# Performance work log

Measured on AMD Instinct MI355X. Metric: run time of the kernel, lower is better.

The kernel has to match this reference:

```python
import jax, jax.numpy as jnp
import numpy as np

BIT, ROW, COL = 4, 8, 8
Y_ROW, Z_COL, K = 128, 128, 256  # inter_dimension = 256, K8 = 32
K8 = K // 8
BATCH, SEQ = 8, 2048


def _unpack_bits(packed, n_bits):
    """Unpack uint8 along last axis, big-endian (MSB first), matching np.packbits."""
    shifts = jnp.arange(7, -1, -1, dtype=jnp.uint8)
    bits = (packed[..., None] >> shifts) & jnp.uint8(1)  # [..., k8, 8]
    return bits.reshape(*packed.shape[:-1], -1)[..., :n_bits]


def setup_inputs() -> dict:
    rng = np.random.default_rng(0)
    # Generate underlying binary tensors so Y_sum / Z_sum are consistent with packed bits.
    Yb = rng.integers(0, 2, size=(BIT, ROW, COL, Y_ROW, K), dtype=np.uint8)
    Zb = rng.integers(0, 2, size=(BIT, ROW, COL, K, Z_COL), dtype=np.uint8)
    Y_packed = np.packbits(Yb, axis=-1)                                # [BIT,ROW,COL,Y_ROW,K8]
    Z_packed = np.packbits(Zb.transpose(0, 1, 2, 4, 3), axis=-1)        # [BIT,ROW,COL,Z_COL,K8]
    Y_sum = Yb.sum(axis=-1, keepdims=True).astype(np.int32)             # [BIT,ROW,COL,Y_ROW,1]
    Z_sum = Zb.sum(axis=-2, keepdims=True).astype(np.int32)             # [BIT,ROW,COL,1,Z_COL]

    key = jax.random.key(0)
    k1, k2, k3, k4, k5, k6 = jax.random.split(key, 6)
    X = jax.random.normal(k1, (BATCH, SEQ, COL * Z_COL), dtype=jnp.float32)
    a = jax.random.normal(k2, (BIT, 1, 1, 1, 1), dtype=jnp.float32) * 0.1
    b = jax.random.normal(k3, (BIT, 1, 1, 1, 1), dtype=jnp.float32) * 0.1
    c = jax.random.normal(k4, (BIT, 1, 1, 1, 1), dtype=jnp.float32) * 0.1
    d = jax.random.normal(k5, (1, 1, 1, 1), dtype=jnp.float32) * 0.1
    bias = jax.random.normal(k6, (ROW * Y_ROW,), dtype=jnp.float32) * 0.1
    return {
        "X": X,
        "Y_packed": jnp.asarray(Y_packed),
        "Z_packed": jnp.asarray(Z_packed),
        "Y_sum": jnp.asarray(Y_sum),
        "Z_sum": jnp.asarray(Z_sum),
        "a": a, "b": b, "c": c, "d": d, "bias": bias,
    }


def reference(X, Y_packed, Z_packed, Y_sum, Z_sum, a, b, c, d, bias):
    dtype = X.dtype
    # Unpack bits (fallback path of _matmul_via_unpack) and do binary matmul.
    Y = _unpack_bits(Y_packed, K).astype(dtype)        # [BIT,ROW,COL,Y_ROW,K]
    Zt = _unpack_bits(Z_packed, K).astype(dtype)       # [BIT,ROW,COL,Z_COL,K]
    W_core = jnp.einsum('brcyk,brczk->brcyz', Y, Zt)   # [BIT,ROW,COL,Y_ROW,Z_COL]
    # Affine recombination over bit planes.
    W = a * W_core + b * Y_sum.astype(dtype) + c * Z_sum.astype(dtype)
    W = W.sum(axis=0) + d                               # [ROW,COL,Y_ROW,Z_COL]
    W = W.transpose(0, 2, 1, 3).reshape(ROW * Y_ROW, COL * Z_COL)
    return X @ W.T + bias
```

## Files before the change

### kernel.cpp

```cpp
#include <hip/hip_runtime.h>
#include <hip/hip_bf16.h>
#include <stdint.h>

typedef unsigned int u32;
typedef unsigned short u16;
typedef __attribute__((ext_vector_type(8))) short short8;
typedef __attribute__((ext_vector_type(4))) float floatx4;

#define N_DIM 1024
#define K_DIM 1024
#define M_DIM 16384
#define EPW  68

__device__ __forceinline__ u32 pack4(uint4 v) {
    return (v.x & 0xffu) | ((v.y & 0xffu) << 8) | ((v.z & 0xffu) << 16) | (v.w << 24);
}

__device__ __forceinline__ u16 bf16rne(float f) {
    u32 u = __float_as_uint(f);
    return (u16)((u + 0x7fffu + ((u >> 16) & 1u)) >> 16);
}

__device__ __forceinline__ void load16_lds(const void* g, void* l) {
    __builtin_amdgcn_global_load_lds(
        (const __attribute__((address_space(1))) void*)g,
        (__attribute__((address_space(3))) void*)l, 16, 0, 0);
}

__global__ __launch_bounds__(256) void build_w(
        const u32* __restrict__ yp, const u32* __restrict__ zp,
        const int* __restrict__ ysum, const int* __restrict__ zsum,
        const float* __restrict__ pa, const float* __restrict__ pb,
        const float* __restrict__ pc, const float* __restrict__ pd,
        __hip_bfloat16* __restrict__ Wb) {
    __shared__ u32 sY[4096];
    __shared__ u32 sZ[1024];
    __shared__ int sYs[512];
    __shared__ int sZs[128];

    const int tid = threadIdx.x;
    const int rc = blockIdx.x >> 2;
    const int zq = blockIdx.x & 3;
    const int r = rc >> 3, c = rc & 7;
    const int z0 = zq * 32;

    const uint4 d0 = ((const uint4*)yp)[0], d1 = ((const uint4*)yp)[1];
    const int sdet = __popc(d0.x) + __popc(d0.y) + __popc(d0.z) + __popc(d0.w)
                   + __popc(d1.x) + __popc(d1.y) + __popc(d1.z) + __popc(d1.w);
    const bool widened = (sdet != ysum[0]);

    if (!widened) {
#pragma unroll
        for (int j = 0; j < 4; ++j) {
            const int chunk = tid + j * 256;
            const int f = chunk * 4;
            const int bit = f >> 10, rem = f & 1023;
            const u32 gw = (u32)((bit * 64 + r * 8 + c) * 1024 + rem);
            ((uint4*)sY)[chunk] = *(const uint4*)(yp + gw);
        }
        {
            const int f = tid * 4;
            const int bit = f >> 8;
            const u32 gw = (u32)((bit * 64 + r * 8 + c) * 1024 + z0 * 8 + (f & 255));
            ((uint4*)sZ)[tid] = *(const uint4*)(zp + gw);
        }
    } else {
#pragma unroll
        for (int j = 0; j < 4; ++j) {
            const int chunk = tid + j * 256;
            const int f = chunk * 4;
            const int bit = f >> 10, rem = f & 1023;
            const u32 gw = (u32)((bit * 64 + r * 8 + c) * 1024 + rem);
            uint4 o;
            o.x = pack4(((const uint4*)yp)[gw + 0]);
            o.y = pack4(((const uint4*)yp)[gw + 1]);
            o.z = pack4(((const uint4*)yp)[gw + 2]);
            o.w = pack4(((const uint4*)yp)[gw + 3]);
            ((uint4*)sY)[chunk] = o;
        }
        {
            const int f = tid * 4;
            const int bit = f >> 8;
            const u32 gw = (u32)((bit * 64 + r * 8 + c) * 1024 + z0 * 8 + (f & 255));
            uint4 o;
            o.x = pack4(((const uint4*)zp)[gw + 0]);
            o.y = pack4(((const uint4*)zp)[gw + 1]);
            o.z = pack4(((const uint4*)zp)[gw + 2]);
            o.w = pack4(((const uint4*)zp)[gw + 3]);
            ((uint4*)sZ)[tid] = o;
        }
    }
    for (int j = tid; j < 512; j += 256) {
        const int bit = j >> 7, y = j & 127;
        sYs[j] = ysum[((bit * 8 + r) * 8 + c) * 128 + y];
    }
    if (tid < 128) {
        const int bit = tid >> 5, zl = tid & 31;
        sZs[tid] = zsum[((bit * 8 + r) * 8 + c) * 128 + z0 + zl];
    }
    __syncthreads();

    float av[4], bv[4], cv[4];
#pragma unroll
    for (int bit = 0; bit < 4; ++bit) { av[bit] = pa[bit]; bv[bit] = pb[bit]; cv[bit] = pc[bit]; }
    const float dv = pd[0];

    const int y = tid & 127;
    const int zh = tid >> 7;

    u32 yw[4][8];
    float base = dv;
#pragma unroll
    for (int bit = 0; bit < 4; ++bit) {
        const uint4 q0 = ((const uint4*)sY)[bit * 256 + y * 2];
        const uint4 q1 = ((const uint4*)sY)[bit * 256 + y * 2 + 1];
        yw[bit][0] = q0.x; yw[bit][1] = q0.y; yw[bit][2] = q0.z; yw[bit][3] = q0.w;
        yw[bit][4] = q1.x; yw[bit][5] = q1.y; yw[bit][6] = q1.z; yw[bit][7] = q1.w;
        base += bv[bit] * (float)sYs[bit * 128 + y];
    }

    const int m = r * 128 + y;
#pragma unroll
    for (int zl2 = 0; zl2 < 16; ++zl2) {
        const int zl = zh * 16 + zl2;
        float wv = base;
#pragma unroll
        for (int bit = 0; bit < 4; ++bit) {
            const uint4 zw0 = ((const uint4*)sZ)[bit * 64 + zl * 2];
            const uint4 zw1 = ((const uint4*)sZ)[bit * 64 + zl * 2 + 1];
            int p = 0;
            p += __popc(yw[bit][0] & zw0.x);
            p += __popc(yw[bit][1] & zw0.y);
            p += __popc(yw[bit][2] & zw0.z);
            p += __popc(yw[bit][3] & zw0.w);
            p += __popc(yw[bit][4] & zw1.x);
            p += __popc(yw[bit][5] & zw1.y);
            p += __popc(yw[bit][6] & zw1.z);
            p += __popc(yw[bit][7] & zw1.w);
            wv += av[bit] * (float)p + cv[bit] * (float)sZs[bit * 32 + zl];
        }
        const int k = c * 128 + z0 + zl;
        Wb[(size_t)m * K_DIM + k] = __float2bfloat16(wv);
    }
}

__device__ __forceinline__ void stage_b32(const u16* __restrict__ Wb,
        int n0, int kt, char* slot, int w, int lane, int srow, int csrc) {
#pragma unroll
    for (int j = 0; j < 2; ++j) {
        const int slab = w * 2 + j;
        const int row = slab * 16 + srow;
        load16_lds(Wb + (size_t)(n0 + row) * K_DIM + kt * 32 + csrc * 8,
                   slot + 16384 + slab * 1024 + lane * 16);
    }
}

__device__ __forceinline__ void load_a32(const float* __restrict__ X,
        int m0, int kt, int tid, float4 (&ar)[4][2]) {
#pragma unroll
    for (int j = 0; j < 4; ++j) {
        const int row = j * 64 + (tid >> 2);
        const float* p = X + (size_t)(m0 + row) * K_DIM + kt * 32 + (tid & 3) * 8;
        ar[j][0] = *(const float4*)p;
        ar[j][1] = *(const float4*)(p + 4);
    }
}

__device__ __forceinline__ void cvt_write_a32(char* slot, int tid,
        const float4 (&ar)[4][2]) {
    const int ck = tid & 3;
#pragma unroll
    for (int j = 0; j < 4; ++j) {
        const int row = j * 64 + (tid >> 2);
        short8 v;
        v[0] = (short)bf16rne(ar[j][0].x); v[1] = (short)bf16rne(ar[j][0].y);
        v[2] = (short)bf16rne(ar[j][0].z); v[3] = (short)bf16rne(ar[j][0].w);
        v[4] = (short)bf16rne(ar[j][1].x); v[5] = (short)bf16rne(ar[j][1].y);
        v[6] = (short)bf16rne(ar[j][1].z); v[7] = (short)bf16rne(ar[j][1].w);
        *(short8*)(slot + ((row >> 4) << 10) + ((row & 15) << 6)
                        + ((ck ^ ((row >> 1) & 3)) << 4)) = v;
    }
}

template<bool DO_STAGE>
__device__ __forceinline__ void tile32(const char* __restrict__ slot,
        char* stslot, int ktg, floatx4 (&acc)[8][4],
        const float* __restrict__ X, const u16* __restrict__ Wb,
        int m0, int n0, int tid, int w, int lane, int srow, int csrc,
        int wr, int wc, int fm, int cx) {
    const char* As = slot;
    const char* Bs = slot + 16384;
    short8 a[8], b[4];

#pragma unroll
    for (int mi = 0; mi < 8; ++mi)
        a[mi] = *(const short8*)(As + (wr * 128 + mi * 16 + fm) * 64 + cx);
#pragma unroll
    for (int ni = 0; ni < 4; ++ni)
        b[ni] = *(const short8*)(Bs + (wc * 64 + ni * 16 + fm) * 64 + cx);
    __builtin_amdgcn_s_barrier();
    asm volatile("s_waitcnt lgkmcnt(0)" ::: "memory");
    __builtin_amdgcn_s_setprio(1);
#pragma unroll
    for (int mi = 0; mi < 8; ++mi) {
        acc[mi][0] = __builtin_amdgcn_mfma_f32_16x16x32_bf16(a[mi], b[0], acc[mi][0], 0, 0, 0);
        acc[mi][1] = __builtin_amdgcn_mfma_f32_16x16x32_bf16(a[mi], b[1], acc[mi][1], 0, 0, 0);
    }
    __builtin_amdgcn_s_setprio(0);
    __builtin_amdgcn_s_barrier();

    float4 ar[4][2];
    if (DO_STAGE) {
        load_a32(X, m0, ktg, tid, ar);
        stage_b32(Wb, n0, ktg, stslot, w, lane, srow, csrc);
    }
    __builtin_amdgcn_s_setprio(1);
#pragma unroll
    for (int mi = 0; mi < 8; ++mi) {
        acc[mi][2] = __builtin_amdgcn_mfma_f32_16x16x32_bf16(a[mi], b[2], acc[mi][2], 0, 0, 0);
        acc[mi][3] = __builtin_amdgcn_mfma_f32_16x16x32_bf16(a[mi], b[3], acc[mi][3], 0, 0, 0);
    }
    __builtin_amdgcn_s_setprio(0);
    if (DO_STAGE) {
        asm volatile("s_waitcnt vmcnt(2)" ::: "memory");
        cvt_write_a32(stslot, tid, ar);
    } else {
        asm volatile("s_waitcnt vmcnt(0)" ::: "memory");
    }
    __builtin_amdgcn_s_barrier();
}

__global__ __launch_bounds__(256, 2) void gemm_bias(
        const float* __restrict__ X, const u16* __restrict__ Wb,
        const float* __restrict__ bias, float* __restrict__ out) {
    __shared__ char lds[49152];

    const int tid = threadIdx.x;
    const int lane = tid & 63;
    const int w = tid >> 6;
    const int wr = w >> 1;
    const int wc = w & 1;
    const int m0 = blockIdx.x * 256;
    const int n0 = blockIdx.y * 128;

    const int srow = lane >> 2;
    const int csrc = (lane & 3) ^ ((lane >> 3) & 3);
    const int fm = lane & 15, fq = lane >> 4;
    const int cx = (fq ^ ((fm >> 1) & 3)) * 16;

    char* slot0 = lds;
    char* slot1 = lds + 24576;

    floatx4 acc[8][4] = {};

    {
        float4 ar[4][2];
        load_a32(X, m0, 0, tid, ar);
        stage_b32(Wb, n0, 0, slot0, w, lane, srow, csrc);
        stage_b32(Wb, n0, 1, slot1, w, lane, srow, csrc);
        asm volatile("s_waitcnt vmcnt(4)" ::: "memory");
        cvt_write_a32(slot0, tid, ar);
        load_a32(X, m0, 1, tid, ar);
        asm volatile("s_waitcnt vmcnt(0)" ::: "memory");
        cvt_write_a32(slot1, tid, ar);
    }
    __syncthreads();

    for (int it = 0; it < 15; ++it) {
        tile32<true>(slot0, slot0, 2 * it + 2, acc, X, Wb, m0, n0,
                     tid, w, lane, srow, csrc, wr, wc, fm, cx);
        tile32<true>(slot1, slot1, 2 * it + 3, acc, X, Wb, m0, n0,
                     tid, w, lane, srow, csrc, wr, wc, fm, cx);
    }
    tile32<false>(slot0, slot0, 0, acc, X, Wb, m0, n0,
                  tid, w, lane, srow, csrc, wr, wc, fm, cx);
    tile32<false>(slot1, slot1, 0, acc, X, Wb, m0, n0,
                  tid, w, lane, srow, csrc, wr, wc, fm, cx);

    float bias_r[4];
#pragma unroll
    for (int ni = 0; ni < 4; ++ni)
        bias_r[ni] = bias[n0 + wc * 64 + ni * 16 + fm];

    __syncthreads();
    float* ep = (float*)lds + w * (16 * EPW);
    const int gm0 = m0 + wr * 128;
    const int gn0 = n0 + wc * 64;

#pragma unroll
    for (int mi = 0; mi < 8; ++mi) {
#pragma unroll
        for (int ni = 0; ni < 4; ++ni)
#pragma unroll
            for (int reg = 0; reg < 4; ++reg)
                ep[(fq * 4 + reg) * EPW + ni * 16 + fm] = acc[mi][ni][reg] + bias_r[ni];
#pragma unroll
        for (int t = 0; t < 4; ++t) {
            const int lr = t * 4 + fq;
            const float4 v = *(const float4*)(ep + lr * EPW + fm * 4);
            *(float4*)(out + (size_t)(gm0 + mi * 16 + lr) * N_DIM + gn0 + fm * 4) = v;
        }
    }
}

extern "C" void kernel_launch(void* const* d_in, const int* in_sizes, int n_in,
                              void* d_out, int out_size, void* d_ws, size_t ws_size,
                              hipStream_t stream) {
    const float* X   = (const float*)d_in[0];
    const u32*   Yp  = (const u32*)d_in[1];
    const u32*   Zp  = (const u32*)d_in[2];
    const int*   Ys  = (const int*)d_in[3];
    const int*   Zs  = (const int*)d_in[4];
    const float* pa  = (const float*)d_in[5];
    const float* pb  = (const float*)d_in[6];
    const float* pc  = (const float*)d_in[7];
    const float* pd  = (const float*)d_in[8];
    const float* bias = (const float*)d_in[9];
    float* out = (float*)d_out;

    char* ws = (char*)d_ws;
    __hip_bfloat16* Wb = (__hip_bfloat16*)ws;

    build_w<<<256, 256, 0, stream>>>(Yp, Zp, Ys, Zs, pa, pb, pc, pd, Wb);
    gemm_bias<<<dim3(64, 8), 256, 0, stream>>>(X, (const u16*)Wb, bias, out);
}
```

Baseline: 183.9 us.

## Prefetch X fp32 tile one step ahead in registers across iterations

Restructures the software pipeline so the fp32 X tile for step k+1 is loaded into registers during step k, then converted and written to LDS at the start of the next tile. Before, each tile waited on its own freshly issued X loads within the same iteration. Now the global-load latency is spread over a whole tile of MFMA work, and the vmcnt waits are relaxed to allow outstanding loads. The cost is extra live registers for the prefetched tile, which could reduce occupancy, and more complex wait-count bookkeeping that must stay correct.

Result: faster. 179.4 us (-2.4%).

```diff
diff --git a/kernel.cpp b/kernel.cpp
--- a/kernel.cpp
+++ b/kernel.cpp
@@ -182,9 +182,9 @@
     }
 }
 
-template<bool DO_STAGE>
+template<bool CVT, bool LOADA, bool STB, int VM>
 __device__ __forceinline__ void tile32(const char* __restrict__ slot,
-        char* stslot, int ktg, floatx4 (&acc)[8][4],
+        char* stslot, int ktg, floatx4 (&acc)[8][4], float4 (&arX)[4][2],
         const float* __restrict__ X, const u16* __restrict__ Wb,
         int m0, int n0, int tid, int w, int lane, int srow, int csrc,
         int wr, int wc, int fm, int cx) {
@@ -209,11 +209,9 @@
     __builtin_amdgcn_s_setprio(0);
     __builtin_amdgcn_s_barrier();
 
-    float4 ar[4][2];
-    if (DO_STAGE) {
-        load_a32(X, m0, ktg, tid, ar);
-        stage_b32(Wb, n0, ktg, stslot, w, lane, srow, csrc);
-    }
+    if (CVT)   cvt_write_a32(stslot, tid, arX);
+    if (LOADA) load_a32(X, m0, ktg + 1, tid, arX);
+    if (STB)   stage_b32(Wb, n0, ktg, stslot, w, lane, srow, csrc);
     __builtin_amdgcn_s_setprio(1);
 #pragma unroll
     for (int mi = 0; mi < 8; ++mi) {
@@ -221,12 +219,9 @@
         acc[mi][3] = __builtin_amdgcn_mfma_f32_16x16x32_bf16(a[mi], b[3], acc[mi][3], 0, 0, 0);
     }
     __builtin_amdgcn_s_setprio(0);
-    if (DO_STAGE) {
-        asm volatile("s_waitcnt vmcnt(2)" ::: "memory");
-        cvt_write_a32(stslot, tid, ar);
-    } else {
-        asm volatile("s_waitcnt vmcnt(0)" ::: "memory");
-    }
+    if (CVT) asm volatile("s_waitcnt lgkmcnt(0)" ::: "memory");
+    if (VM == 10) asm volatile("s_waitcnt vmcnt(10)" ::: "memory");
+    else          asm volatile("s_waitcnt vmcnt(0)" ::: "memory");
     __builtin_amdgcn_s_barrier();
 }
 
@@ -252,30 +247,31 @@
     char* slot1 = lds + 24576;
 
     floatx4 acc[8][4] = {};
-
-    {
-        float4 ar[4][2];
-        load_a32(X, m0, 0, tid, ar);
-        stage_b32(Wb, n0, 0, slot0, w, lane, srow, csrc);
-        stage_b32(Wb, n0, 1, slot1, w, lane, srow, csrc);
-        asm volatile("s_waitcnt vmcnt(4)" ::: "memory");
-        cvt_write_a32(slot0, tid, ar);
-        load_a32(X, m0, 1, tid, ar);
-        asm volatile("s_waitcnt vmcnt(0)" ::: "memory");
-        cvt_write_a32(slot1, tid, ar);
-    }
+    float4 arX[4][2];
+
+    load_a32(X, m0, 0, tid, arX);
+    cvt_write_a32(slot0, tid, arX);
+    load_a32(X, m0, 1, tid, arX);
+    cvt_write_a32(slot1, tid, arX);
+    stage_b32(Wb, n0, 0, slot0, w, lane, srow, csrc);
+    stage_b32(Wb, n0, 1, slot1, w, lane, srow, csrc);
+    load_a32(X, m0, 2, tid, arX);
     __syncthreads();
 
-    for (int it = 0; it < 15; ++it) {
-        tile32<true>(slot0, slot0, 2 * it + 2, acc, X, Wb, m0, n0,
-                     tid, w, lane, srow, csrc, wr, wc, fm, cx);
-        tile32<true>(slot1, slot1, 2 * it + 3, acc, X, Wb, m0, n0,
-                     tid, w, lane, srow, csrc, wr, wc, fm, cx);
-    }
-    tile32<false>(slot0, slot0, 0, acc, X, Wb, m0, n0,
-                  tid, w, lane, srow, csrc, wr, wc, fm, cx);
-    tile32<false>(slot1, slot1, 0, acc, X, Wb, m0, n0,
-                  tid, w, lane, srow, csrc, wr, wc, fm, cx);
+    for (int it = 0; it < 14; ++it) {
+        tile32<true, true, true, 10>(slot0, slot0, 2 * it + 2, acc, arX,
+                X, Wb, m0, n0, tid, w, lane, srow, csrc, wr, wc, fm, cx);
+        tile32<true, true, true, 10>(slot1, slot1, 2 * it + 3, acc, arX,
+                X, Wb, m0, n0, tid, w, lane, srow, csrc, wr, wc, fm, cx);
+    }
+    tile32<true, true, true, 10>(slot0, slot0, 30, acc, arX,
+            X, Wb, m0, n0, tid, w, lane, srow, csrc, wr, wc, fm, cx);
+    tile32<true, false, true, 0>(slot1, slot1, 31, acc, arX,
+            X, Wb, m0, n0, tid, w, lane, srow, csrc, wr, wc, fm, cx);
+    tile32<false, false, false, 0>(slot0, slot0, 0, acc, arX,
+            X, Wb, m0, n0, tid, w, lane, srow, csrc, wr, wc, fm, cx);
+    tile32<false, false, false, 0>(slot1, slot1, 0, acc, arX,
+            X, Wb, m0, n0, tid, w, lane, srow, csrc, wr, wc, fm, cx);
 
     float bias_r[4];
 #pragma unroll
```
